# Performance work log

Measured on AMD Instinct MI355X. Metric: run time of the kernel, lower is better.

The kernel has to match this reference:

```python
import jax, jax.numpy as jnp
import numpy as np

B, S, E, H, L, DFF = 2, 2048, 512, 8, 2, 2048
D = E // H
EPS = 1e-5


def layernorm(x, g, b):
    mu = jnp.mean(x, axis=-1, keepdims=True)
    var = jnp.var(x, axis=-1, keepdims=True)
    return (x - mu) * jax.lax.rsqrt(var + EPS) * g + b


def layernorm_noaffine(x):
    mu = jnp.mean(x, axis=-1, keepdims=True)
    var = jnp.var(x, axis=-1, keepdims=True)
    return (x - mu) * jax.lax.rsqrt(var + EPS)


def setup_inputs() -> dict:
    key = jax.random.key(0)
    ks = jax.random.split(key, 16)
    s = 0.02
    inp = {
        "x": jax.random.normal(ks[0], (B, S, E), dtype=jnp.float32),
        "mask": jax.random.randint(ks[1], (B, S), 0, 2) == 1,
        # per-layer attention projections, stacked over layers
        "wq": jax.random.normal(ks[2], (L, E, E), dtype=jnp.float32) * s,
        "bq": jnp.zeros((L, E), dtype=jnp.float32),
        "wk": jax.random.normal(ks[3], (L, E, E), dtype=jnp.float32) * s,
        "bk": jnp.zeros((L, E), dtype=jnp.float32),
        "wv": jax.random.normal(ks[4], (L, E, E), dtype=jnp.float32) * s,
        "bv": jnp.zeros((L, E), dtype=jnp.float32),
        # shared norms (module defines a single norm1/norm2 used by every layer)
        "g1": jnp.ones((E,), dtype=jnp.float32),
        "b1": jnp.zeros((E,), dtype=jnp.float32),
        "g2": jnp.ones((E,), dtype=jnp.float32),
        "b2": jnp.zeros((E,), dtype=jnp.float32),
        "gf": jnp.ones((E,), dtype=jnp.float32),
        "bf": jnp.zeros((E,), dtype=jnp.float32),
        # shared Dense FFN (single self.dense used after every layer)
        "W1": jax.random.normal(ks[5], (DFF, E), dtype=jnp.float32) * s,
        "B1": jnp.zeros((DFF,), dtype=jnp.float32),
        "W2": jax.random.normal(ks[6], (E, DFF), dtype=jnp.float32) * s,
        "B2": jnp.zeros((E,), dtype=jnp.float32),
    }
    return inp


def _forward(x, wq, bq, wk, bk, wv, bv, g1, b1, g2, b2, gf, bf, W1, B1, W2, B2, mask):
    scale = 1.0 / jnp.sqrt(jnp.float32(D))
    m = mask[:, None, None, :]  # [B,1,1,S] key padding mask, True = pad
    neg_inf = jnp.float32(-jnp.inf)
    for i in range(L):
        h = layernorm(x, g1, b1)  # norm1(x), used for q,k,v
        q = (h @ wq[i].T + bq[i]).reshape(B, S, H, D).transpose(0, 2, 1, 3)
        k = (h @ wk[i].T + bk[i]).reshape(B, S, H, D).transpose(0, 2, 1, 3)
        v = (h @ wv[i].T + bv[i]).reshape(B, S, H, D).transpose(0, 2, 1, 3)
        logits = jnp.einsum("bhqd,bhkd->bhqk", q, k) * scale
        att = jax.nn.softmax(jnp.where(m, neg_inf, logits), axis=-1)
        att = jnp.where(m, 0.0, att)
        out = jnp.einsum("bhqk,bhkd->bhqd", att, v)
        out = out.transpose(0, 2, 1, 3).reshape(B, S, E)
        x = x + layernorm(out, g2, b2)
        # Dense: LayerNorm(no affine) -> Linear -> ReLU -> Linear, residual
        d = layernorm_noaffine(x)
        d = jax.nn.relu(d @ W1.T + B1)
        d = d @ W2.T + B2
        x = x + d
    return layernorm(x, gf, bf)


def reference(x, mask, wq, bq, wk, bk, wv, bv, g1, b1, g2, b2, gf, bf, W1, B1, W2, B2):
    return _forward(x, wq, bq, wk, bk, wv, bv, g1, b1, g2, b2, gf, bf, W1, B1, W2, B2, mask)
```

## Files before the change

kernel.cpp:

```cpp
#include <hip/hip_runtime.h>
#include <hip/hip_bf16.h>

constexpr int BB   = 2;
constexpr int SS   = 2048;
constexpr int EE   = 512;
constexpr int HH   = 8;
constexpr int DD   = 64;
constexpr int DFF_ = 2048;
constexpr int NTOK = BB * SS;
constexpr int NE   = NTOK * EE;
constexpr float EPSF  = 1e-5f;
constexpr float SCL2  = 0.125f * 1.44269504088896f;
constexpr float MBIAS = -1e30f;
constexpr int KSPLIT = 2;
constexpr int KHALF  = SS / KSPLIT;

typedef __bf16 v8bf __attribute__((ext_vector_type(8)));
typedef __bf16 v4bf __attribute__((ext_vector_type(4)));
typedef float  v4f  __attribute__((ext_vector_type(4)));

__device__ __forceinline__ float bf2f(unsigned short u) {
    return __uint_as_float(((unsigned int)u) << 16);
}
__device__ __forceinline__ float bf2f(__bf16 u) {
    unsigned short us = __builtin_bit_cast(unsigned short, u);
    return __uint_as_float(((unsigned int)us) << 16);
}
__device__ __forceinline__ float ldA(const void* p, size_t i, int f) {
    return f ? ((const float*)p)[i] : bf2f(((const unsigned short*)p)[i]);
}
__device__ __forceinline__ void gll16(const void* g, void* l) {
    __builtin_amdgcn_global_load_lds(
        (const __attribute__((address_space(1))) void*)g,
        (__attribute__((address_space(3))) void*)l, 16, 0, 0);
}

__global__ void sniff_kernel(const unsigned short* __restrict__ x, int* flag) {
    __shared__ int cnt[256];
    int t = threadIdx.x, bad = 0;
    for (int i = t; i < 4096; i += 256) {
        float v = bf2f(x[i]);
        if (!(fabsf(v) < 1000.f)) bad++;
    }
    cnt[t] = bad;
    __syncthreads();
    if (t == 0) {
        int s = 0;
        for (int i = 0; i < 256; ++i) s += cnt[i];
        *flag = (s > 8) ? 1 : 0;
    }
}

__global__ void cvt_kernel(const void* __restrict__ in, float* __restrict__ out,
                           int n, const int* __restrict__ flagp) {
    const int f = *flagp;
    int i = (blockIdx.x * blockDim.x + threadIdx.x) * 4;
    if (i >= n) return;
    if (f) {
        *(float4*)(out + i) = *(const float4*)((const float*)in + i);
    } else {
        ushort4 u = *(const ushort4*)((const unsigned short*)in + i);
        out[i + 0] = bf2f(u.x); out[i + 1] = bf2f(u.y);
        out[i + 2] = bf2f(u.z); out[i + 3] = bf2f(u.w);
    }
}

__global__ void wcvt_all(const void* __restrict__ wq, const void* __restrict__ wk,
                         const void* __restrict__ wv, const void* __restrict__ W1,
                         const void* __restrict__ W2, __bf16* __restrict__ out,
                         const int* __restrict__ flagp) {
    const int f = *flagp;
    const int i = (blockIdx.x * blockDim.x + threadIdx.x) * 8;
    constexpr int n1 = 2 * EE * EE;
    constexpr int nf = DFF_ * EE;
    const void* src; int off;
    if      (i < n1)          { src = wq; off = i; }
    else if (i < 2 * n1)      { src = wk; off = i - n1; }
    else if (i < 3 * n1)      { src = wv; off = i - 2 * n1; }
    else if (i < 3 * n1 + nf) { src = W1; off = i - 3 * n1; }
    else                      { src = W2; off = i - 3 * n1 - nf; }
    if (f) {
        const float* p = (const float*)src + off;
        #pragma unroll
        for (int j = 0; j < 8; ++j) out[i + j] = (__bf16)p[j];
    } else {
        *(uint4*)(out + i) = *(const uint4*)((const unsigned short*)src + off);
    }
}

__global__ __launch_bounds__(256) void ln_kernel(
    const float* __restrict__ src,
    const void* __restrict__ g, const void* __restrict__ b,
    __bf16* __restrict__ dstb, void* __restrict__ outp,
    const int* __restrict__ flagp)
{
    const int f = *flagp;
    const int row = blockIdx.x, t = threadIdx.x;
    const float* x = src + (size_t)row * EE;
    float v0 = x[t], v1 = x[t + 256];
    float s = v0 + v1, q = v0 * v0 + v1 * v1;
    #pragma unroll
    for (int off = 32; off > 0; off >>= 1) {
        s += __shfl_down(s, off, 64);
        q += __shfl_down(q, off, 64);
    }
    __shared__ float red[8], st[2];
    const int wid = t >> 6;
    if ((t & 63) == 0) { red[wid] = s; red[4 + wid] = q; }
    __syncthreads();
    if (t == 0) {
        float S_ = red[0] + red[1] + red[2] + red[3];
        float Q_ = red[4] + red[5] + red[6] + red[7];
        float mu = S_ / EE;
        st[0] = mu;
        st[1] = rsqrtf(Q_ / EE - mu * mu + EPSF);
    }
    __syncthreads();
    const float mu = st[0], rs = st[1];
    float o0 = (v0 - mu) * rs, o1 = (v1 - mu) * rs;
    if (g) {
        o0 = o0 * ldA(g, t, f)       + ldA(b, t, f);
        o1 = o1 * ldA(g, t + 256, f) + ldA(b, t + 256, f);
    }
    const size_t i0 = (size_t)row * EE + t, i1 = i0 + 256;
    if (dstb) { dstb[i0] = (__bf16)o0; dstb[i1] = (__bf16)o1; }
    if (outp) {
        if (f) { ((float*)outp)[i0] = o0; ((float*)outp)[i1] = o1; }
        else {
            ((__hip_bfloat16*)outp)[i0] = __float2bfloat16(o0);
            ((__hip_bfloat16*)outp)[i1] = __float2bfloat16(o1);
        }
    }
}

__global__ __launch_bounds__(256) void combine_ln(
    const __bf16* __restrict__ Opart, const float* __restrict__ MLl,
    const void* __restrict__ g2, const void* __restrict__ b2,
    float* __restrict__ X, __bf16* __restrict__ Hb,
    const int* __restrict__ flagp)
{
    const int f = *flagp;
    const int tok = blockIdx.x, t = threadIdx.x;
    const int b = tok >> 11, s_ = tok & 2047;
    __shared__ float cinv[8];
    __shared__ float red[8], st[2];
    if (t < 8) {
        const size_t r0 = (size_t)(b * 8 + t) * SS + s_;
        const size_t r1 = (size_t)(16 + b * 8 + t) * SS + s_;
        float l = MLl[r0] + MLl[r1];
        cinv[t] = (l > 0.f) ? 1.f / l : 0.f;
    }
    __syncthreads();
    float a0, a1;
    {
        int c = t, h = c >> 6, d = c & 63;
        size_t p0 = ((size_t)(b * 8 + h) * SS + s_) * 64 + d;
        size_t p1 = ((size_t)(16 + b * 8 + h) * SS + s_) * 64 + d;
        a0 = (bf2f(Opart[p0]) + bf2f(Opart[p1])) * cinv[h];
        c = t + 256; h = c >> 6; d = c & 63;
        p0 = ((size_t)(b * 8 + h) * SS + s_) * 64 + d;
        p1 = ((size_t)(16 + b * 8 + h) * SS + s_) * 64 + d;
        a1 = (bf2f(Opart[p0]) + bf2f(Opart[p1])) * cinv[h];
    }
    const int wid = t >> 6;
    {
        float s = a0 + a1, q = a0 * a0 + a1 * a1;
        #pragma unroll
        for (int off = 32; off > 0; off >>= 1) {
            s += __shfl_down(s, off, 64);
            q += __shfl_down(q, off, 64);
        }
        if ((t & 63) == 0) { red[wid] = s; red[4 + wid] = q; }
    }
    __syncthreads();
    if (t == 0) {
        float S_ = red[0] + red[1] + red[2] + red[3];
        float Q_ = red[4] + red[5] + red[6] + red[7];
        float mu = S_ / EE;
        st[0] = mu;
        st[1] = rsqrtf(Q_ / EE - mu * mu + EPSF);
    }
    __syncthreads();
    const float mu1 = st[0], rs1 = st[1];
    const size_t i0 = (size_t)tok * EE + t, i1 = i0 + 256;
    float l0v = (a0 - mu1) * rs1 * ldA(g2, t, f)       + ldA(b2, t, f);
    float l1v = (a1 - mu1) * rs1 * ldA(g2, t + 256, f) + ldA(b2, t + 256, f);
    float x0 = X[i0] + l0v, x1 = X[i1] + l1v;
    __syncthreads();
    {
        float s = x0 + x1, q = x0 * x0 + x1 * x1;
        #pragma unroll
        for (int off = 32; off > 0; off >>= 1) {
            s += __shfl_down(s, off, 64);
            q += __shfl_down(q, off, 64);
        }
        if ((t & 63) == 0) { red[wid] = s; red[4 + wid] = q; }
    }
    __syncthreads();
    if (t == 0) {
        float S_ = red[0] + red[1] + red[2] + red[3];
        float Q_ = red[4] + red[5] + red[6] + red[7];
        float mu = S_ / EE;
        st[0] = mu;
        st[1] = rsqrtf(Q_ / EE - mu * mu + EPSF);
    }
    __syncthreads();
    const float mu2 = st[0], rs2 = st[1];
    X[i0] = x0; X[i1] = x1;
    Hb[i0] = (__bf16)((x0 - mu2) * rs2);
    Hb[i1] = (__bf16)((x1 - mu2) * rs2);
}

__global__ __launch_bounds__(256) void gemm_mfma(
    const __bf16* __restrict__ A,
    const __bf16* Wa, const __bf16* Wb, const __bf16* Wc,
    const void* ba, const void* bb, const void* bc,
    __bf16* oa, __bf16* ob, __bf16* oc,
    float* __restrict__ Cf,
    int M, int N, int K, int flags,
    size_t welem_off, size_t belem_off, const int* __restrict__ flagp)
{
    const int f = *flagp;
    const int z = blockIdx.z;
    const __bf16* W = (z == 0) ? Wa : (z == 1) ? Wb : Wc;
    const void* bias = (z == 0) ? ba : (z == 1) ? bb : bc;
    __bf16* Cb = (z == 0) ? oa : (z == 1) ? ob : oc;
    W += welem_off;
    int kbeg = 0, kend = K;
    if (flags & 4) {
        const int ks = K >> 2;
        kbeg = z * ks; kend = kbeg + ks;
        if (z != 0) bias = nullptr;
    }

    __shared__ __bf16 As[64 * 32];
    __shared__ __bf16 Bs[128 * 32];
    const int t = threadIdx.x;
    const int w = t >> 6, lane = t & 63;
    const int quad = lane >> 4, l16 = lane & 15;
    const int wr = w >> 1, wc = w & 1;
    const int bm = blockIdx.x * 64, bn = blockIdx.y * 128;

    v4f acc[2][4] = {};
    const int ra = t >> 2, ea = (t & 3) * 8;
    const int c0 = t, c1 = t + 256;
    const int rb0 = c0 >> 2, eb0 = (c0 & 3) * 8;
    const int rb1 = c1 >> 2, eb1 = (c1 & 3) * 8;

    for (int k0 = kbeg; k0 < kend; k0 += 32) {
        __syncthreads();
        gll16(A + (size_t)(bm + ra) * K + k0 + ea,  (char*)As + t * 16);
        gll16(W + (size_t)(bn + rb0) * K + k0 + eb0, (char*)Bs + c0 * 16);
        gll16(W + (size_t)(bn + rb1) * K + k0 + eb1, (char*)Bs + c1 * 16);
        __syncthreads();
        v8bf af[2], bfr[4];
        #pragma unroll
        for (int i = 0; i < 2; ++i) {
            int row = wr * 32 + i * 16 + l16;
            af[i] = *(const v8bf*)&As[row * 32 + quad * 8];
        }
        #pragma unroll
        for (int j = 0; j < 4; ++j) {
            int row = wc * 64 + j * 16 + l16;
            bfr[j] = *(const v8bf*)&Bs[row * 32 + quad * 8];
        }
        #pragma unroll
        for (int i = 0; i < 2; ++i)
            #pragma unroll
            for (int j = 0; j < 4; ++j)
                acc[i][j] = __builtin_amdgcn_mfma_f32_16x16x32_bf16(
                    af[i], bfr[j], acc[i][j], 0, 0, 0);
    }

    float bvv[4];
    #pragma unroll
    for (int j = 0; j < 4; ++j) {
        int col = bn + wc * 64 + j * 16 + l16;
        bvv[j] = bias ? ldA(bias, belem_off + col, f) : 0.f;
    }

    if ((flags & 8) && z == 2) {
        #pragma unroll
        for (int i = 0; i < 2; ++i) {
            const int row0 = bm + wr * 32 + i * 16 + quad * 4;
            const int b_ = row0 >> 11, s_ = row0 & 2047;
            #pragma unroll
            for (int j = 0; j < 4; ++j) {
                const int col = bn + wc * 64 + j * 16 + l16;
                const int h_ = col >> 6, d_ = col & 63;
                v4bf u;
                #pragma unroll
                for (int r = 0; r < 4; ++r) u[r] = (__bf16)(acc[i][j][r] + bvv[j]);
                *(v4bf*)(Cb + ((size_t)((b_ * 8 + h_) * 64 + d_)) * SS + s_) = u;
            }
        }
        return;
    }

    #pragma unroll
    for (int i = 0; i < 2; ++i) {
        const int rowb = bm + wr * 32 + i * 16 + quad * 4;
        #pragma unroll
        for (int j = 0; j < 4; ++j) {
            const int col = bn + wc * 64 + j * 16 + l16;
            #pragma unroll
            for (int r = 0; r < 4; ++r) {
                float v = acc[i][j][r] + bvv[j];
                if (flags & 1) v = fmaxf(v, 0.f);
                const size_t idx = (size_t)(rowb + r) * N + col;
                if (flags & 4)      unsafeAtomicAdd(&Cf[idx], v);
                else if (flags & 2) Cf[idx] += v;
                else                Cb[idx] = (__bf16)v;
            }
        }
    }
}

__global__ __launch_bounds__(256) void attn_mfma(
    const __bf16* __restrict__ Qg, const __bf16* __restrict__ Kg,
    const __bf16* __restrict__ Vtg, const int* __restrict__ mask,
    __bf16* __restrict__ Opart, float* __restrict__ MLl)
{
    __shared__ __bf16 Ks[64][88];
    __shared__ __bf16 Vs[64][88];
    __shared__ __bf16 Ps[4][16][72];
    __shared__ float  mkf[64];

    const int t = threadIdx.x;
    const int w = t >> 6, lane = t & 63;
    const int quad = lane >> 4, l16 = lane & 15;
    const int bh = blockIdx.y, b = bh >> 3, h = bh & 7;
    const int q0 = blockIdx.x * 64;
    const int z  = blockIdx.z;
    const int kof = z * KHALF;

    const __bf16* qrow = Qg + ((size_t)(b * SS + q0 + w * 16 + l16)) * EE + h * DD + quad * 8;
    const v8bf qa0 = *(const v8bf*)qrow;
    const v8bf qa1 = *(const v8bf*)(qrow + 32);

    const int lr = t >> 2, lc = (t & 3) * 16;
    const __bf16* kbase = Kg  + ((size_t)(b * SS + kof + lr)) * EE + h * DD + lc;
    const __bf16* vbase = Vtg + ((size_t)((b * 8 + h) * 64 + lr)) * SS + kof + lc;

    v8bf ka  = *(const v8bf*)kbase;
    v8bf kb2 = *(const v8bf*)(kbase + 8);
    v8bf va  = *(const v8bf*)vbase;
    v8bf vb2 = *(const v8bf*)(vbase + 8);
    float mb = 0.f;
    if (t < 64) mb = mask[b * SS + kof + t] ? MBIAS : 0.f;

    float l_acc = 0.f;
    v4f o[4] = {};

    for (int k0 = 0; k0 < KHALF; k0 += 64) {
        *(v8bf*)&Ks[lr][lc]     = ka;
        *(v8bf*)&Ks[lr][lc + 8] = kb2;
        *(v8bf*)&Vs[lr][lc]     = va;
        *(v8bf*)&Vs[lr][lc + 8] = vb2;
        if (t < 64) mkf[t] = mb;
        __syncthreads();
        if (k0 + 64 < KHALF) {
            const __bf16* kp = kbase + (size_t)(k0 + 64) * EE;
            const __bf16* vp = vbase + (k0 + 64);
            ka  = *(const v8bf*)kp;
            kb2 = *(const v8bf*)(kp + 8);
            va  = *(const v8bf*)vp;
            vb2 = *(const v8bf*)(vp + 8);
            if (t < 64) mb = mask[b * SS + kof + k0 + 64 + t] ? MBIAS : 0.f;
        }

        v4f s4[4];
        #pragma unroll
        for (int j = 0; j < 4; ++j) {
            v8bf kf0 = *(const v8bf*)&Ks[j * 16 + l16][quad * 8];
            v8bf kf1 = *(const v8bf*)&Ks[j * 16 + l16][32 + quad * 8];
            v4f zz = {};
            zz = __builtin_amdgcn_mfma_f32_16x16x32_bf16(kf0, qa0, zz, 0, 0, 0);
            zz = __builtin_amdgcn_mfma_f32_16x16x32_bf16(kf1, qa1, zz, 0, 0, 0);
            s4[j] = zz;
        }
        float4 mk4[4];
        #pragma unroll
        for (int j = 0; j < 4; ++j) mk4[j] = *(const float4*)&mkf[j * 16 + quad * 4];

        float ts = 0.f;
        #pragma unroll
        for (int j = 0; j < 4; ++j) {
            float p0 = exp2f(fmaf(s4[j][0], SCL2, mk4[j].x));
            float p1 = exp2f(fmaf(s4[j][1], SCL2, mk4[j].y));
            float p2 = exp2f(fmaf(s4[j][2], SCL2, mk4[j].z));
            float p3 = exp2f(fmaf(s4[j][3], SCL2, mk4[j].w));
            ts += (p0 + p1) + (p2 + p3);
            v4bf u;
            u[0] = (__bf16)p0; u[1] = (__bf16)p1;
            u[2] = (__bf16)p2; u[3] = (__bf16)p3;
            *(v4bf*)&Ps[w][l16][j * 16 + quad * 4] = u;
        }
        l_acc += ts;

        v8bf pb0 = *(const v8bf*)&Ps[w][l16][quad * 8];
        v8bf pb1 = *(const v8bf*)&Ps[w][l16][32 + quad * 8];
        #pragma unroll
        for (int dt = 0; dt < 4; ++dt) {
            v8bf vf0 = *(const v8bf*)&Vs[dt * 16 + l16][quad * 8];
            v8bf vf1 = *(const v8bf*)&Vs[dt * 16 + l16][32 + quad * 8];
            o[dt] = __builtin_amdgcn_mfma_f32_16x16x32_bf16(vf0, pb0, o[dt], 0, 0, 0);
            o[dt] = __builtin_amdgcn_mfma_f32_16x16x32_bf16(vf1, pb1, o[dt], 0, 0, 0);
        }
        __syncthreads();
    }

    l_acc += __shfl_xor(l_acc, 16, 64);
    l_acc += __shfl_xor(l_acc, 32, 64);

    const size_t qi = (size_t)(z * 16 + bh) * SS + (q0 + w * 16 + l16);
    __bf16* op = Opart + qi * 64;
    #pragma unroll
    for (int dt = 0; dt < 4; ++dt) {
        v4bf u;
        #pragma unroll
        for (int r = 0; r < 4; ++r) u[r] = (__bf16)o[dt][r];
        *(v4bf*)(op + dt * 16 + quad * 4) = u;
    }
    if (quad == 0) MLl[qi] = l_acc;
}

extern "C" void kernel_launch(void* const* d_in, const int* in_sizes, int n_in,
                              void* d_out, int out_size, void* d_ws, size_t ws_size,
                              hipStream_t stream) {
    const void* x_in = d_in[0];
    const int*  mask = (const int*)d_in[1];
    const void* wq = d_in[2];  const void* bq = d_in[3];
    const void* wk = d_in[4];  const void* bk = d_in[5];
    const void* wv = d_in[6];  const void* bv = d_in[7];
    const void* g1 = d_in[8];  const void* b1 = d_in[9];
    const void* g2 = d_in[10]; const void* b2 = d_in[11];
    const void* gf = d_in[12]; const void* bfp= d_in[13];
    const void* W1 = d_in[14]; const void* B1 = d_in[15];
    const void* W2 = d_in[16]; const void* B2 = d_in[17];

    float* base = (float*)d_ws;
    int*   flag = (int*)base;
    float* X   = base + 16;
    float* AO  = X + NE;
    float* fQ  = AO + NE;
    float* fK  = fQ + NE / 2;
    float* fV  = fK + NE / 2;
    float* fH  = fV + NE / 2;
    float* fW  = fH + NE / 2;
    __bf16* Qb    = (__bf16*)fQ;
    __bf16* Kb    = (__bf16*)fK;
    __bf16* Vtg   = (__bf16*)fV;
    __bf16* Hb    = (__bf16*)fH;
    __bf16* MID   = (__bf16*)AO;
    __bf16* Opart = (__bf16*)AO;
    __bf16* wqc = (__bf16*)fW;
    __bf16* wkc = wqc + 2 * EE * EE;
    __bf16* wvc = wkc + 2 * EE * EE;
    __bf16* W1c = wvc + 2 * EE * EE;
    __bf16* W2c = W1c + DFF_ * EE;
    float* MLl = (float*)(W2c + (size_t)EE * DFF_);

    sniff_kernel<<<1, 256, 0, stream>>>((const unsigned short*)x_in, flag);
    cvt_kernel<<<NE / 4 / 256, 256, 0, stream>>>(x_in, X, NE, flag);
    wcvt_all<<<1792, 256, 0, stream>>>(wq, wk, wv, W1, W2, wqc, flag);

    const dim3 gQKV(NTOK / 64, EE / 128, 3);
    const dim3 gF1 (NTOK / 64, DFF_ / 128, 1);
    const dim3 gF2 (NTOK / 64, EE / 128, 4);
    const dim3 gAtt(SS / 64, BB * HH, KSPLIT);

    for (int l = 0; l < 2; ++l) {
        const size_t wo = (size_t)l * EE * EE, bo = (size_t)l * EE;
        ln_kernel<<<NTOK, 256, 0, stream>>>(X, g1, b1, Hb, nullptr, flag);
        gemm_mfma<<<gQKV, 256, 0, stream>>>(Hb, wqc, wkc, wvc, bq, bk, bv,
            Qb, Kb, Vtg, nullptr, NTOK, EE, EE, 8, wo, bo, flag);
        attn_mfma<<<gAtt, 256, 0, stream>>>(Qb, Kb, Vtg, mask, Opart, MLl);
        combine_ln<<<NTOK, 256, 0, stream>>>(Opart, MLl, g2, b2, X, Hb, flag);
        gemm_mfma<<<gF1, 256, 0, stream>>>(Hb, W1c, W1c, W1c, B1, B1, B1,
            MID, MID, MID, nullptr, NTOK, DFF_, EE, 1, 0, 0, flag);
        gemm_mfma<<<gF2, 256, 0, stream>>>(MID, W2c, W2c, W2c, B2, B2, B2,
            nullptr, nullptr, nullptr, X, NTOK, EE, DFF_, 2 | 4, 0, 0, flag);
    }
    ln_kernel<<<NTOK, 256, 0, stream>>>(X, gf, bfp, nullptr, d_out, flag);
}
```

Measured before the change: 371.3 us.

## Double-buffer GEMM LDS tiles and keep attention probabilities in registers via permuted V layout

The GEMM kernel now uses two LDS buffers and prefetches the next K-slice while computing the current one, dropping one barrier per iteration. The V-transpose epilogue writes sequence positions in a permuted order within each 64-block, so the attention kernel can pack softmax probabilities straight into MFMA B-operand registers instead of round-tripping them through shared memory. This removes the Ps LDS buffer and its store/load traffic. The price is doubled GEMM LDS use and reliance on the permutation matching the MFMA accumulator layout exactly.

```diff
diff --git a/kernel.cpp b/kernel.cpp
--- a/kernel.cpp
+++ b/kernel.cpp
@@ -233,8 +233,8 @@
         if (z != 0) bias = nullptr;
     }
 
-    __shared__ __bf16 As[64 * 32];
-    __shared__ __bf16 Bs[128 * 32];
+    __shared__ __bf16 As[2][64 * 32];
+    __shared__ __bf16 Bs[2][128 * 32];
     const int t = threadIdx.x;
     const int w = t >> 6, lane = t & 63;
     const int quad = lane >> 4, l16 = lane & 15;
@@ -247,22 +247,29 @@
     const int rb0 = c0 >> 2, eb0 = (c0 & 3) * 8;
     const int rb1 = c1 >> 2, eb1 = (c1 & 3) * 8;
 
+    gll16(A + (size_t)(bm + ra) * K + kbeg + ea,  (char*)As[0] + t * 16);
+    gll16(W + (size_t)(bn + rb0) * K + kbeg + eb0, (char*)Bs[0] + c0 * 16);
+    gll16(W + (size_t)(bn + rb1) * K + kbeg + eb1, (char*)Bs[0] + c1 * 16);
+
+    int p = 0;
     for (int k0 = kbeg; k0 < kend; k0 += 32) {
         __syncthreads();
-        gll16(A + (size_t)(bm + ra) * K + k0 + ea,  (char*)As + t * 16);
-        gll16(W + (size_t)(bn + rb0) * K + k0 + eb0, (char*)Bs + c0 * 16);
-        gll16(W + (size_t)(bn + rb1) * K + k0 + eb1, (char*)Bs + c1 * 16);
-        __syncthreads();
+        if (k0 + 32 < kend) {
+            const int kn = k0 + 32, q_ = p ^ 1;
+            gll16(A + (size_t)(bm + ra) * K + kn + ea,  (char*)As[q_] + t * 16);
+            gll16(W + (size_t)(bn + rb0) * K + kn + eb0, (char*)Bs[q_] + c0 * 16);
+            gll16(W + (size_t)(bn + rb1) * K + kn + eb1, (char*)Bs[q_] + c1 * 16);
+        }
         v8bf af[2], bfr[4];
         #pragma unroll
         for (int i = 0; i < 2; ++i) {
             int row = wr * 32 + i * 16 + l16;
-            af[i] = *(const v8bf*)&As[row * 32 + quad * 8];
+            af[i] = *(const v8bf*)&As[p][row * 32 + quad * 8];
         }
         #pragma unroll
         for (int j = 0; j < 4; ++j) {
             int row = wc * 64 + j * 16 + l16;
-            bfr[j] = *(const v8bf*)&Bs[row * 32 + quad * 8];
+            bfr[j] = *(const v8bf*)&Bs[p][row * 32 + quad * 8];
         }
         #pragma unroll
         for (int i = 0; i < 2; ++i)
@@ -270,6 +277,7 @@
             for (int j = 0; j < 4; ++j)
                 acc[i][j] = __builtin_amdgcn_mfma_f32_16x16x32_bf16(
                     af[i], bfr[j], acc[i][j], 0, 0, 0);
+        p ^= 1;
     }
 
     float bvv[4];
@@ -283,7 +291,9 @@
         #pragma unroll
         for (int i = 0; i < 2; ++i) {
             const int row0 = bm + wr * 32 + i * 16 + quad * 4;
-            const int b_ = row0 >> 11, s_ = row0 & 2047;
+            const int b_ = row0 >> 11, sl = row0 & 2047;
+            const int s64 = sl & ~63, sloc = sl & 63;
+            const int slot = (sloc & 32) + ((sloc >> 2) & 3) * 8 + ((sloc >> 4) & 1) * 4;
             #pragma unroll
             for (int j = 0; j < 4; ++j) {
                 const int col = bn + wc * 64 + j * 16 + l16;
@@ -291,7 +301,7 @@
                 v4bf u;
                 #pragma unroll
                 for (int r = 0; r < 4; ++r) u[r] = (__bf16)(acc[i][j][r] + bvv[j]);
-                *(v4bf*)(Cb + ((size_t)((b_ * 8 + h_) * 64 + d_)) * SS + s_) = u;
+                *(v4bf*)(Cb + ((size_t)((b_ * 8 + h_) * 64 + d_)) * SS + s64 + slot) = u;
             }
         }
         return;
@@ -323,7 +333,6 @@
 {
     __shared__ __bf16 Ks[64][88];
     __shared__ __bf16 Vs[64][88];
-    __shared__ __bf16 Ps[4][16][72];
     __shared__ float  mkf[64];
 
     const int t = threadIdx.x;
@@ -383,6 +392,7 @@
         #pragma unroll
         for (int j = 0; j < 4; ++j) mk4[j] = *(const float4*)&mkf[j * 16 + quad * 4];
 
+        v8bf pb0, pb1;
         float ts = 0.f;
         #pragma unroll
         for (int j = 0; j < 4; ++j) {
@@ -391,15 +401,16 @@
             float p2 = exp2f(fmaf(s4[j][2], SCL2, mk4[j].z));
             float p3 = exp2f(fmaf(s4[j][3], SCL2, mk4[j].w));
             ts += (p0 + p1) + (p2 + p3);
-            v4bf u;
-            u[0] = (__bf16)p0; u[1] = (__bf16)p1;
-            u[2] = (__bf16)p2; u[3] = (__bf16)p3;
-            *(v4bf*)&Ps[w][l16][j * 16 + quad * 4] = u;
+            if (j < 2) {
+                pb0[j * 4 + 0] = (__bf16)p0; pb0[j * 4 + 1] = (__bf16)p1;
+                pb0[j * 4 + 2] = (__bf16)p2; pb0[j * 4 + 3] = (__bf16)p3;
+            } else {
+                pb1[(j - 2) * 4 + 0] = (__bf16)p0; pb1[(j - 2) * 4 + 1] = (__bf16)p1;
+                pb1[(j - 2) * 4 + 2] = (__bf16)p2; pb1[(j - 2) * 4 + 3] = (__bf16)p3;
+            }
         }
         l_acc += ts;
 
-        v8bf pb0 = *(const v8bf*)&Ps[w][l16][quad * 8];
-        v8bf pb1 = *(const v8bf*)&Ps[w][l16][32 + quad * 8];
         #pragma unroll
         for (int dt = 0; dt < 4; ++dt) {
             v8bf vf0 = *(const v8bf*)&Vs[dt * 16 + l16][quad * 8];
```

Result: no change. 370.1 us (-0.3%).
